# Optimization experiments

Hardware: AMD Instinct MI355X
Metric: run time of the kernel (lower is better)

The kernel has to match this reference:

```python
import jax, jax.numpy as jnp
import numpy as np

B, N, E = 4, 512, 128
NODE_F, EDGE_F, DYN_F, L = 16, 8, 6, 3
TOT_F = NODE_F + DYN_F  # 22


def setup_inputs() -> dict:
    key = jax.random.key(0)
    ks = jax.random.split(key, 20)
    s = 0.05
    return {
        "node_features": jax.random.normal(ks[0], (B, N, NODE_F), jnp.float32),
        "edge_features": jax.random.normal(ks[1], (B, N, N, EDGE_F), jnp.float32),
        "W": jax.random.normal(ks[2], (B, N, N), jnp.float32),
        "assigned": jax.random.randint(ks[3], (B, N), 0, 2) > 0,
        "open_group": jax.random.randint(ks[4], (B, N), 0, 2) > 0,
        "action_mask": jax.random.randint(ks[5], (B, N), 0, 2) > 0,
        "build_limit": jax.random.uniform(ks[6], (B, 3), jnp.float32, 0.5, 2.0),
        "open_group_size": jax.random.uniform(ks[7], (B, 3), jnp.float32, 0.0, 2.0),
        "node_embed_w": jax.random.normal(ks[8], (TOT_F, E), jnp.float32) * s,
        "node_embed_b": jnp.zeros((E,), jnp.float32),
        "mp_node_w": jax.random.normal(ks[9], (L, E, E), jnp.float32) * s,
        "mp_edge_w": jax.random.normal(ks[10], (L, EDGE_F, E), jnp.float32) * s,
        "mp_weight_w": jax.random.normal(ks[11], (L, E), jnp.float32) * s,
        "mp_out_w": jax.random.normal(ks[12], (L, E, E), jnp.float32) * s,
        "mp_out_b": jnp.zeros((L, E), jnp.float32),
        "context_w": jax.random.normal(ks[13], (E, E), jnp.float32) * s,
        "key_w": jax.random.normal(ks[14], (E, E), jnp.float32) * s,
        "logit_bias": jnp.zeros((1,), jnp.float32),
    }


def _policy_logits(node_features, edge_features, W, build_limit, open_group_size,
                   node_embed_w, node_embed_b, mp_node_w, mp_edge_w, mp_weight_w,
                   mp_out_w, mp_out_b, context_w, key_w, logit_bias,
                   assigned, open_group, action_mask):
    # --- dynamic node features: [B,N,6] ---
    ratio = open_group_size / jnp.maximum(build_limit, 1e-6)  # [B,3]
    dyn = jnp.concatenate([
        assigned.astype(jnp.float32)[..., None],
        open_group.astype(jnp.float32)[..., None],
        action_mask.astype(jnp.float32)[..., None],
        jnp.broadcast_to(ratio[:, None, :], (node_features.shape[0], node_features.shape[1], 3)),
    ], axis=-1)
    x = jnp.concatenate([node_features, dyn], axis=-1)  # [B,N,22]
    h = x @ node_embed_w + node_embed_b  # [B,N,E]

    # --- edge-aware message passing, residual per layer ---
    for l in range(L):
        hi = h @ mp_node_w[l]  # [B,N,E]
        ej = jnp.einsum('bijf,fe->bije', edge_features, mp_edge_w[l])  # [B,N,N,E]
        wij = W[..., None] * mp_weight_w[l]  # [B,N,N,E]
        msg = jnp.tanh(hi[:, :, None, :] + ej + wij)  # [B,N,N,E]
        agg = msg.mean(axis=2)  # [B,N,E]
        h = h + agg @ mp_out_w[l] + mp_out_b[l]

    # --- context attention logits ---
    og = open_group.astype(jnp.float32)
    has_open = jnp.any(open_group, axis=-1, keepdims=True)  # [B,1]
    denom = jnp.maximum(og.sum(axis=-1, keepdims=True), 1.0)  # [B,1]
    group_mean = (h * og[..., None]).sum(axis=1) / denom  # [B,E]
    sep_emb = h[:, 0, :]
    context = jnp.where(has_open, group_mean, sep_emb)  # [B,E]
    query = context @ context_w  # [B,E]
    keys = h @ key_w  # [B,N,E]
    logits = jnp.einsum('be,bne->bn', query, keys) / jnp.sqrt(jnp.float32(h.shape[-1]))
    logits = logits + logit_bias[0]
    logits = jnp.where(action_mask, logits, -1e9)
    return logits


def reference(node_features, edge_features, W, assigned, open_group, action_mask,
              build_limit, open_group_size, node_embed_w, node_embed_b,
              mp_node_w, mp_edge_w, mp_weight_w, mp_out_w, mp_out_b,
              context_w, key_w, logit_bias):
    return _policy_logits(node_features, edge_features, W, build_limit, open_group_size,
                          node_embed_w, node_embed_b, mp_node_w, mp_edge_w, mp_weight_w,
                          mp_out_w, mp_out_b, context_w, key_w, logit_bias,
                          assigned, open_group, action_mask)
```

## Files before the change

kernel.cpp:

```cpp
#include <hip/hip_runtime.h>
#include <math.h>

#define BB 4
#define NN 512
#define EE 128
#define NODE_F 16
#define EDGE_F 8
#define LL 3

typedef __attribute__((ext_vector_type(8))) short bf16x8;
typedef __attribute__((ext_vector_type(4))) float f32x4;

__device__ __forceinline__ ushort bf_hi(float x) {
    uint u = __float_as_uint(x);
    return (ushort)((u + 0x7fffu + ((u >> 16) & 1u)) >> 16);
}
__device__ __forceinline__ float bf_f(ushort h) {
    return __uint_as_float(((uint)h) << 16);
}

__global__ __launch_bounds__(512) void k_zero(float* __restrict__ gbuf) {
    for (int i = threadIdx.x; i < BB * EE + BB; i += 512)
        gbuf[i] = 0.0f;
}

__global__ __launch_bounds__(512) void k_rows(
    const float* __restrict__ nf,
    const float* __restrict__ ef,
    const float* __restrict__ W,
    const int*   __restrict__ assigned,
    const int*   __restrict__ open_group,
    const int*   __restrict__ action_mask,
    const float* __restrict__ build_limit,
    const float* __restrict__ open_group_size,
    const float* __restrict__ embed_w,
    const float* __restrict__ embed_b,
    const float* __restrict__ node_w,
    const float* __restrict__ edge_w,
    const float* __restrict__ weight_w,
    const float* __restrict__ out_w,
    const float* __restrict__ out_b,
    float* __restrict__ hout,
    float* __restrict__ gsum,
    float* __restrict__ gcnt)
{
    const int i   = blockIdx.x;
    const int b   = blockIdx.y;
    const int t   = threadIdx.x;
    const int l   = t & 63;
    const int w   = t >> 6;
    const int row = b * NN + i;

    __shared__ bf16x8 afr[32 * 64];
    __shared__ float hsh[EE];
    __shared__ float aggfin[EE];
    __shared__ float xsh[24];

    if (t < NODE_F) {
        xsh[t] = nf[row * NODE_F + t];
    } else if (t == 16) {
        xsh[16] = assigned[row] ? 1.0f : 0.0f;
    } else if (t == 17) {
        xsh[17] = open_group[row] ? 1.0f : 0.0f;
    } else if (t == 18) {
        xsh[18] = action_mask[row] ? 1.0f : 0.0f;
    } else if (t < 22) {
        int k = t - 19;
        xsh[t] = open_group_size[b * 3 + k] / fmaxf(build_limit[b * 3 + k], 1e-6f);
    }

    {
        const float* efr = ef + (size_t)row * NN * EDGE_F;
        const float* Wr  = W + (size_t)row * NN;
        #pragma unroll
        for (int q = 0; q < 4; ++q) {
            const int eid = t + 512 * q;
            const int ll  = eid & 63;
            const int jt  = eid >> 6;
            const int g   = ll >> 4;
            const int jj  = jt * 16 + (ll & 15);
            bf16x8 frag;
            if (g < 3) {
                const float4 a = *(const float4*)&efr[jj * 8];
                const float4 c4 = *(const float4*)&efr[jj * 8 + 4];
                float v[8] = {a.x, a.y, a.z, a.w, c4.x, c4.y, c4.z, c4.w};
                if (g < 2) {
                    #pragma unroll
                    for (int m = 0; m < 8; ++m) frag[m] = (short)bf_hi(v[m]);
                } else {
                    #pragma unroll
                    for (int m = 0; m < 8; ++m) {
                        ushort h = bf_hi(v[m]);
                        frag[m] = (short)bf_hi(v[m] - bf_f(h));
                    }
                }
            } else {
                float wv = Wr[jj];
                ushort h = bf_hi(wv);
                ushort lo = bf_hi(wv - bf_f(h));
                frag = (bf16x8){(short)h, (short)h, (short)lo, 0, 0, 0, 0, 0};
            }
            afr[eid] = frag;
        }
    }
    __syncthreads();

    if (t < EE) {
        float h0 = embed_b[t];
        #pragma unroll
        for (int k = 0; k < 22; ++k)
            h0 = fmaf(xsh[k], embed_w[k * EE + t], h0);
        hsh[t] = h0;
    }

    const float c  = 2.8853900817779268f;
    const int  le  = l & 15;
    const int  g   = l >> 4;
    const int  eN  = w * 16 + le;

    for (int lay = 0; lay < LL; ++lay) {
        __syncthreads();

        float hp = 0.0f;
        {
            const float* nw = node_w + lay * EE * EE + g * 32 * EE + eN;
            #pragma unroll
            for (int kk = 0; kk < 2; ++kk) {
                float wreg[16];
                #pragma unroll
                for (int k2 = 0; k2 < 16; ++k2)
                    wreg[k2] = nw[(kk * 16 + k2) * EE];
                #pragma unroll
                for (int k2 = 0; k2 < 16; ++k2)
                    hp = fmaf(hsh[g * 32 + kk * 16 + k2], wreg[k2], hp);
            }
            hp += __shfl_xor(hp, 16);
            hp += __shfl_xor(hp, 32);
        }
        const float hq = c * hp;

        bf16x8 bfrag;
        if (g == 3) {
            float x = c * weight_w[lay * EE + eN];
            ushort h = bf_hi(x);
            ushort lo = bf_hi(x - bf_f(h));
            bfrag = (bf16x8){(short)h, (short)lo, (short)h, 0, 0, 0, 0, 0};
        } else {
            const float* ewp = edge_w + lay * EDGE_F * EE + eN;
            if (g == 1) {
                #pragma unroll
                for (int m = 0; m < 8; ++m) {
                    float x = c * ewp[m * EE];
                    ushort h = bf_hi(x);
                    bfrag[m] = (short)bf_hi(x - bf_f(h));
                }
            } else {
                #pragma unroll
                for (int m = 0; m < 8; ++m)
                    bfrag[m] = (short)bf_hi(c * ewp[m * EE]);
            }
        }

        const f32x4 cin = {hq, hq, hq, hq};

        f32x4 rsum = {0.0f, 0.0f, 0.0f, 0.0f};
        #pragma unroll 4
        for (int jt = 0; jt < 32; ++jt) {
            bf16x8 a = afr[jt * 64 + l];
            f32x4 acc = __builtin_amdgcn_mfma_f32_16x16x32_bf16(a, bfrag, cin, 0, 0, 0);
            #pragma unroll
            for (int r = 0; r < 4; ++r) {
                float ex = __builtin_amdgcn_exp2f(acc[r]);
                rsum[r] += __builtin_amdgcn_rcpf(ex + 1.0f);
            }
        }
        float s = (rsum[0] + rsum[1]) + (rsum[2] + rsum[3]);
        s += __shfl_xor(s, 16);
        s += __shfl_xor(s, 32);
        if (l < 16)
            aggfin[eN] = 1.0f - s * (1.0f / 256.0f);
        __syncthreads();

        float op = 0.0f;
        {
            const float* ow = out_w + lay * EE * EE + g * 32 * EE + eN;
            #pragma unroll
            for (int kk = 0; kk < 2; ++kk) {
                float wreg[16];
                #pragma unroll
                for (int k2 = 0; k2 < 16; ++k2)
                    wreg[k2] = ow[(kk * 16 + k2) * EE];
                #pragma unroll
                for (int k2 = 0; k2 < 16; ++k2)
                    op = fmaf(aggfin[g * 32 + kk * 16 + k2], wreg[k2], op);
            }
            op += __shfl_xor(op, 16);
            op += __shfl_xor(op, 32);
        }
        if (l < 16)
            hsh[eN] = hsh[eN] + out_b[lay * EE + eN] + op;
    }

    __syncthreads();
    if (t < EE) {
        const float hv = hsh[t];
        hout[(size_t)row * EE + t] = hv;
        if (open_group[row]) atomicAdd(&gsum[b * EE + t], hv);
    }
    if (t == 256 && open_group[row]) atomicAdd(&gcnt[b], 1.0f);
}

__global__ __launch_bounds__(128) void k_ctx(
    const float* __restrict__ hbuf,
    const float* __restrict__ gsum,
    const float* __restrict__ gcnt,
    const float* __restrict__ context_w,
    const float* __restrict__ key_w,
    float* __restrict__ qk)
{
    const int b = blockIdx.x;
    const int e = threadIdx.x;

    __shared__ float csh[EE];
    __shared__ float qsh[EE];

    const float cnt = gcnt[b];
    const float ctx = (cnt > 0.0f) ? (gsum[b * EE + e] / fmaxf(cnt, 1.0f))
                                   : hbuf[(size_t)b * NN * EE + e];
    csh[e] = ctx;
    __syncthreads();

    float q = 0.0f;
    #pragma unroll
    for (int kk = 0; kk < 8; ++kk) {
        float wreg[16];
        #pragma unroll
        for (int k2 = 0; k2 < 16; ++k2)
            wreg[k2] = context_w[(kk * 16 + k2) * EE + e];
        #pragma unroll
        for (int k2 = 0; k2 < 16; ++k2)
            q = fmaf(csh[kk * 16 + k2], wreg[k2], q);
    }
    qsh[e] = q;
    __syncthreads();

    float acc = 0.0f;
    const float* kr = key_w + e * EE;
    #pragma unroll
    for (int kk = 0; kk < 8; ++kk) {
        float wreg[16];
        #pragma unroll
        for (int k2 = 0; k2 < 16; ++k2)
            wreg[k2] = kr[kk * 16 + k2];
        #pragma unroll
        for (int k2 = 0; k2 < 16; ++k2)
            acc = fmaf(wreg[k2], qsh[kk * 16 + k2], acc);
    }
    qk[b * EE + e] = acc;
}

__global__ __launch_bounds__(512) void k_logits(
    const float* __restrict__ hbuf,
    const float* __restrict__ qk,
    const int*   __restrict__ action_mask,
    const float* __restrict__ logit_bias,
    float* __restrict__ out)
{
    const int b    = blockIdx.y;
    const int base = blockIdx.x * 32;
    const int wid  = threadIdx.x >> 6;
    const int lane = threadIdx.x & 63;

    const float* hb = hbuf + (size_t)b * NN * EE;
    const float* qb = qk + b * EE;
    const float q0 = qb[lane];
    const float q1 = qb[lane + 64];
    const float lb = logit_bias[0];

    #pragma unroll
    for (int u = 0; u < 4; ++u) {
        const int r = base + wid * 4 + u;
        const float* hr = hb + (size_t)r * EE;
        float p = hr[lane] * q0 + hr[lane + 64] * q1;
        #pragma unroll
        for (int off = 32; off; off >>= 1)
            p += __shfl_down(p, off);
        if (lane == 0) {
            float v = fmaf(p, 0.08838834764831845f, lb);
            out[b * NN + r] = action_mask[b * NN + r] ? v : -1000000000.0f;
        }
    }
}

extern "C" void kernel_launch(void* const* d_in, const int* in_sizes, int n_in,
                              void* d_out, int out_size, void* d_ws, size_t ws_size,
                              hipStream_t stream) {
    const float* nf         = (const float*)d_in[0];
    const float* ef         = (const float*)d_in[1];
    const float* W          = (const float*)d_in[2];
    const int*   assigned   = (const int*)d_in[3];
    const int*   open_group = (const int*)d_in[4];
    const int*   action_mask= (const int*)d_in[5];
    const float* build_limit= (const float*)d_in[6];
    const float* og_size    = (const float*)d_in[7];
    const float* embed_w    = (const float*)d_in[8];
    const float* embed_b    = (const float*)d_in[9];
    const float* node_w     = (const float*)d_in[10];
    const float* edge_w     = (const float*)d_in[11];
    const float* weight_w   = (const float*)d_in[12];
    const float* out_w      = (const float*)d_in[13];
    const float* out_b      = (const float*)d_in[14];
    const float* context_w  = (const float*)d_in[15];
    const float* key_w      = (const float*)d_in[16];
    const float* logit_bias = (const float*)d_in[17];

    float* hbuf = (float*)d_ws;
    float* qk   = hbuf + (size_t)BB * NN * EE;
    float* gbuf = qk + BB * EE;
    float* gsum = gbuf;
    float* gcnt = gbuf + BB * EE;

    k_zero<<<1, 512, 0, stream>>>(gbuf);

    dim3 grid_rows(NN, BB, 1);
    k_rows<<<grid_rows, 512, 0, stream>>>(nf, ef, W, assigned, open_group,
        action_mask, build_limit, og_size, embed_w, embed_b, node_w, edge_w,
        weight_w, out_w, out_b, hbuf, gsum, gcnt);

    k_ctx<<<BB, 128, 0, stream>>>(hbuf, gsum, gcnt, context_w, key_w, qk);

    dim3 grid_log(16, BB, 1);
    k_logits<<<grid_log, 512, 0, stream>>>(hbuf, qk, action_mask, logit_bias,
        (float*)d_out);
}
```

Measured before the change: 220.9 us.

## Fuse context/query computation into logits kernel, drop atomics and zero kernel

Removes the zeroing kernel and the atomic group-sum accumulation in the row kernel. The group mean, query and query-key projections now run redundantly inside each logits block, which reduces four launches to two. In exchange every one of the 64 tail blocks re-reads a full batch of h (512x128) plus both weight matrices, so the tail does more total work.

```diff
diff --git a/kernel.cpp b/kernel.cpp
--- a/kernel.cpp
+++ b/kernel.cpp
@@ -17,11 +17,6 @@
 }
 __device__ __forceinline__ float bf_f(ushort h) {
     return __uint_as_float(((uint)h) << 16);
-}
-
-__global__ __launch_bounds__(512) void k_zero(float* __restrict__ gbuf) {
-    for (int i = threadIdx.x; i < BB * EE + BB; i += 512)
-        gbuf[i] = 0.0f;
 }
 
 __global__ __launch_bounds__(512) void k_rows(
@@ -40,9 +35,7 @@
     const float* __restrict__ weight_w,
     const float* __restrict__ out_w,
     const float* __restrict__ out_b,
-    float* __restrict__ hout,
-    float* __restrict__ gsum,
-    float* __restrict__ gcnt)
+    float* __restrict__ hout)
 {
     const int i   = blockIdx.x;
     const int b   = blockIdx.y;
@@ -202,79 +195,84 @@
     }
 
     __syncthreads();
-    if (t < EE) {
-        const float hv = hsh[t];
-        hout[(size_t)row * EE + t] = hv;
-        if (open_group[row]) atomicAdd(&gsum[b * EE + t], hv);
-    }
-    if (t == 256 && open_group[row]) atomicAdd(&gcnt[b], 1.0f);
-}
-
-__global__ __launch_bounds__(128) void k_ctx(
+    if (t < EE) hout[(size_t)row * EE + t] = hsh[t];
+}
+
+__global__ __launch_bounds__(512) void k_tail2(
     const float* __restrict__ hbuf,
-    const float* __restrict__ gsum,
-    const float* __restrict__ gcnt,
+    const int*   __restrict__ open_group,
     const float* __restrict__ context_w,
     const float* __restrict__ key_w,
-    float* __restrict__ qk)
-{
-    const int b = blockIdx.x;
-    const int e = threadIdx.x;
-
-    __shared__ float csh[EE];
-    __shared__ float qsh[EE];
-
-    const float cnt = gcnt[b];
-    const float ctx = (cnt > 0.0f) ? (gsum[b * EE + e] / fmaxf(cnt, 1.0f))
-                                   : hbuf[(size_t)b * NN * EE + e];
-    csh[e] = ctx;
-    __syncthreads();
-
-    float q = 0.0f;
-    #pragma unroll
-    for (int kk = 0; kk < 8; ++kk) {
-        float wreg[16];
-        #pragma unroll
-        for (int k2 = 0; k2 < 16; ++k2)
-            wreg[k2] = context_w[(kk * 16 + k2) * EE + e];
-        #pragma unroll
-        for (int k2 = 0; k2 < 16; ++k2)
-            q = fmaf(csh[kk * 16 + k2], wreg[k2], q);
-    }
-    qsh[e] = q;
-    __syncthreads();
-
-    float acc = 0.0f;
-    const float* kr = key_w + e * EE;
-    #pragma unroll
-    for (int kk = 0; kk < 8; ++kk) {
-        float wreg[16];
-        #pragma unroll
-        for (int k2 = 0; k2 < 16; ++k2)
-            wreg[k2] = kr[kk * 16 + k2];
-        #pragma unroll
-        for (int k2 = 0; k2 < 16; ++k2)
-            acc = fmaf(wreg[k2], qsh[kk * 16 + k2], acc);
-    }
-    qk[b * EE + e] = acc;
-}
-
-__global__ __launch_bounds__(512) void k_logits(
-    const float* __restrict__ hbuf,
-    const float* __restrict__ qk,
     const int*   __restrict__ action_mask,
     const float* __restrict__ logit_bias,
     float* __restrict__ out)
 {
     const int b    = blockIdx.y;
     const int base = blockIdx.x * 32;
-    const int wid  = threadIdx.x >> 6;
-    const int lane = threadIdx.x & 63;
+    const int t    = threadIdx.x;
+    const int e    = t & 127;
+    const int s    = t >> 7;
+
+    __shared__ float part[4][EE];
+    __shared__ float cnt4[4];
+    __shared__ float csh[EE];
+    __shared__ float qsh[EE];
+    __shared__ float qksh[EE];
 
     const float* hb = hbuf + (size_t)b * NN * EE;
-    const float* qb = qk + b * EE;
-    const float q0 = qb[lane];
-    const float q1 = qb[lane + 64];
+
+    {
+        float gm = 0.0f, cnt = 0.0f;
+        const int n0 = s * 128;
+        #pragma unroll 8
+        for (int u = 0; u < 128; ++u) {
+            const int n = n0 + u;
+            const float m = (float)open_group[b * NN + n];
+            gm = fmaf(m, hb[(size_t)n * EE + e], gm);
+            cnt += m;
+        }
+        part[s][e] = gm;
+        if (e == 0) cnt4[s] = cnt;
+    }
+    __syncthreads();
+
+    if (s == 0) {
+        const float ca = (cnt4[0] + cnt4[1]) + (cnt4[2] + cnt4[3]);
+        const float ga = (part[0][e] + part[1][e]) + (part[2][e] + part[3][e]);
+        csh[e] = (ca > 0.0f) ? (ga / fmaxf(ca, 1.0f)) : hb[e];
+    }
+    __syncthreads();
+
+    {
+        const float* cw = context_w + s * 32 * EE + e;
+        float q = 0.0f;
+        #pragma unroll
+        for (int k = 0; k < 32; ++k)
+            q = fmaf(csh[s * 32 + k], cw[k * EE], q);
+        part[s][e] = q;
+    }
+    __syncthreads();
+    if (s == 0)
+        qsh[e] = (part[0][e] + part[1][e]) + (part[2][e] + part[3][e]);
+    __syncthreads();
+
+    {
+        const float* kr = key_w + e * EE + s * 32;
+        float a = 0.0f;
+        #pragma unroll
+        for (int k = 0; k < 32; ++k)
+            a = fmaf(kr[k], qsh[s * 32 + k], a);
+        part[s][e] = a;
+    }
+    __syncthreads();
+    if (s == 0)
+        qksh[e] = (part[0][e] + part[1][e]) + (part[2][e] + part[3][e]);
+    __syncthreads();
+
+    const int wid  = t >> 6;
+    const int lane = t & 63;
+    const float q0 = qksh[lane];
+    const float q1 = qksh[lane + 64];
     const float lb = logit_bias[0];
 
     #pragma unroll
@@ -315,21 +313,13 @@
     const float* logit_bias = (const float*)d_in[17];
 
     float* hbuf = (float*)d_ws;
-    float* qk   = hbuf + (size_t)BB * NN * EE;
-    float* gbuf = qk + BB * EE;
-    float* gsum = gbuf;
-    float* gcnt = gbuf + BB * EE;
-
-    k_zero<<<1, 512, 0, stream>>>(gbuf);
 
     dim3 grid_rows(NN, BB, 1);
     k_rows<<<grid_rows, 512, 0, stream>>>(nf, ef, W, assigned, open_group,
         action_mask, build_limit, og_size, embed_w, embed_b, node_w, edge_w,
-        weight_w, out_w, out_b, hbuf, gsum, gcnt);
-
-    k_ctx<<<BB, 128, 0, stream>>>(hbuf, gsum, gcnt, context_w, key_w, qk);
-
-    dim3 grid_log(16, BB, 1);
-    k_logits<<<grid_log, 512, 0, stream>>>(hbuf, qk, action_mask, logit_bias,
-        (float*)d_out);
-}
+        weight_w, out_w, out_b, hbuf);
+
+    dim3 grid_tail(16, BB, 1);
+    k_tail2<<<grid_tail, 512, 0, stream>>>(hbuf, open_group, context_w, key_w,
+        action_mask, logit_bias, (float*)d_out);
+}
```

Result: no change. 218.9 us (-0.9%).
